# Optimization experiments

Measured on AMD Instinct MI355X. Metric: run time of the kernel, lower is better.

The kernel has to match this reference:

```python
import jax, jax.numpy as jnp
import numpy as np

EPS = 1e-7  # keras backend.epsilon()
NUM_ROUTING = 3


def squash(v, axis=-1):
    s2 = jnp.sum(jnp.square(v), axis=axis, keepdims=True)
    scale = s2 / (1.0 + s2) / jnp.sqrt(s2 + EPS)
    return scale * v


def setup_inputs() -> dict:
    key = jax.random.key(0)
    k1, k2 = jax.random.split(key)
    B, J, I, P, Q = 64, 32, 2048, 32, 16
    inputs = jax.random.normal(k1, (B, I, Q), dtype=jnp.float32)
    # glorot_uniform for W [J, I, P, Q]
    fan_in, fan_out = Q, P
    limit = np.sqrt(6.0 / (fan_in + fan_out))
    W = jax.random.uniform(k2, (J, I, P, Q), dtype=jnp.float32, minval=-limit, maxval=limit)
    return {"inputs": inputs, "W": W}


def reference(inputs, W):
    # prediction vectors: u_hat[b,j,i,p] = sum_q inputs[b,i,q] * W[j,i,p,q]
    inputs_hat = jnp.einsum('biq,jipq->bjip', inputs, W)  # [B,J,I,P]
    inputs_hat_stop = jax.lax.stop_gradient(inputs_hat)
    B, J, I, _ = inputs_hat.shape
    b = jnp.zeros((B, J, I), dtype=inputs_hat.dtype)
    for _ in range(NUM_ROUTING - 1):
        c = jax.nn.softmax(b, axis=1)  # softmax over output capsules j
        v = squash(jnp.einsum('bji,bjip->bjp', c, inputs_hat_stop))
        b = b + jnp.einsum('bjp,bjip->bji', v, inputs_hat_stop)
    c = jax.nn.softmax(b, axis=1)
    return squash(jnp.einsum('bji,bjip->bjp', c, inputs_hat))  # [B,J,P]
```

## Files before the change

### kernel.cpp

```cpp
#include <hip/hip_runtime.h>


namespace {

using bfrag = __attribute__((ext_vector_type(8))) short;
using ffrag = __attribute__((ext_vector_type(4))) float;

constexpr int I_DIM = 2048;
constexpr int B_DIM = 64;
constexpr int N_DIM = 1024;
constexpr int TI    = 16;

__device__ __forceinline__ unsigned short f2bf(float f) {
    unsigned int u = __float_as_uint(f);
    return (unsigned short)((u + 0x7fffu + ((u >> 16) & 1u)) >> 16);
}

template<int CTRL>
__device__ __forceinline__ float dppf(float x) {
    return __int_as_float(
        __builtin_amdgcn_update_dpp(0, __float_as_int(x), CTRL, 0xF, 0xF, true));
}
__device__ __forceinline__ float sum16(float x) {
    x += dppf<0x121>(x); x += dppf<0x122>(x);
    x += dppf<0x124>(x); x += dppf<0x128>(x);
    return x;
}
__device__ __forceinline__ float max16(float x) {
    x = fmaxf(x, dppf<0x121>(x)); x = fmaxf(x, dppf<0x122>(x));
    x = fmaxf(x, dppf<0x124>(x)); x = fmaxf(x, dppf<0x128>(x));
    return x;
}

__device__ __forceinline__ void gl2lds16(const void* gsrc, void* ldst) {
    __builtin_amdgcn_global_load_lds(
        (const __attribute__((address_space(1))) void*)gsrc,
        (__attribute__((address_space(3))) void*)ldst, 16, 0, 0);
}

__device__ __forceinline__ void barrier_lgkm() {
    asm volatile("s_waitcnt lgkmcnt(0)" ::: "memory");
    __builtin_amdgcn_s_barrier();
    __builtin_amdgcn_sched_barrier(0);
}


__global__ __launch_bounds__(256)
void conv_w(const float* __restrict__ W, unsigned short* __restrict__ Wt) {
    const int t = blockIdx.x * 256 + threadIdx.x;
    const int i = t >> 10, n = t & 1023;
    const float* src = W + ((((n >> 5) * I_DIM + i) * 32 + (n & 31)) << 4);
    unsigned int o[8];
    #pragma unroll
    for (int k = 0; k < 8; ++k)
        o[k] = (unsigned int)f2bf(src[2 * k]) | ((unsigned int)f2bf(src[2 * k + 1]) << 16);
    uint4* d0 = reinterpret_cast<uint4*>(Wt + (((size_t)i * 2 + 0) * 1024 + n) * 8);
    uint4* d1 = reinterpret_cast<uint4*>(Wt + (((size_t)i * 2 + 1) * 1024 + n) * 8);
    *d0 = make_uint4(o[0], o[1], o[2], o[3]);
    *d1 = make_uint4(o[4], o[5], o[6], o[7]);
}

__global__ __launch_bounds__(256)
void conv_x(const float* __restrict__ x, unsigned short* __restrict__ xT2) {
    const int t = blockIdx.x * 256 + threadIdx.x;
    const int i = t >> 6, b = t & 63;
    const float* src = x + (((size_t)b * I_DIM + i) << 4);
    unsigned int o[16];
    #pragma unroll
    for (int k = 0; k < 8; ++k) {
        const float f0 = src[2 * k], f1 = src[2 * k + 1];
        const unsigned short h0 = f2bf(f0), h1 = f2bf(f1);
        const float l0 = f0 - __uint_as_float(((unsigned int)h0) << 16);
        const float l1 = f1 - __uint_as_float(((unsigned int)h1) << 16);
        o[k]     = (unsigned int)h0       | ((unsigned int)h1 << 16);
        o[8 + k] = (unsigned int)f2bf(l0) | ((unsigned int)f2bf(l1) << 16);
    }
    #pragma unroll
    for (int g = 0; g < 4; ++g) {
        uint4* dst = reinterpret_cast<uint4*>(xT2 + (((size_t)i * 4 + g) * 64 + b) * 8);
        *dst = make_uint4(o[4 * g], o[4 * g + 1], o[4 * g + 2], o[4 * g + 3]);
    }
}

#define WAITC() do { if (w == 7) asm volatile("s_waitcnt vmcnt(5)" ::: "memory"); \
                     else        asm volatile("s_waitcnt vmcnt(4)" ::: "memory"); } while (0)

template<int ROUTED>
__global__ __launch_bounds__(512, 2)
void caps_fused(const unsigned short* __restrict__ Wt,
                const unsigned short* __restrict__ xT2,
                const float* __restrict__ v_in,
                float* __restrict__ s_out)
{
    __shared__ short wbuf[2][16384];
    __shared__ short xbuf[2][512];
    __shared__ float d_buf[16 * 36];
    __shared__ float c_buf[16 * 36];

    const int tid = threadIdx.x;
    const int w   = tid >> 6;
    const int l   = tid & 63;
    const int g   = l >> 4;
    const int li  = l & 15;
    const int j0  = w << 2;

    const int bid = (int)blockIdx.x;
    const int V   = (bid & 7) * 64 + (bid >> 3);
    const int it  = V >> 2;
    const int b0  = (V & 3) << 4;
    const int i0  = it * TI;

    float vr[4][8];
    if (ROUTED) {
        #pragma unroll
        for (int r = 0; r < 4; ++r)
            #pragma unroll
            for (int t = 0; t < 8; ++t)
                vr[r][t] = v_in[((b0 + (g << 2) + r) * 32 + j0 + (t >> 1)) * 32
                                + ((t & 1) << 4) + li];
        asm volatile("s_waitcnt vmcnt(0)" ::: "memory");
    }

    auto stage = [&](int i, int bufn) {
        const unsigned short* wsrc = Wt + ((size_t)i << 14);
        #pragma unroll
        for (int k = 0; k < 4; ++k) {
            const int c = (w << 2) + k;
            gl2lds16(wsrc + (c << 9) + (l << 3), &wbuf[bufn][c << 9]);
        }
        if (w == 7)
            gl2lds16(xT2 + (((size_t)i << 2) + (l >> 4)) * 512 + ((b0 + (l & 15)) << 3),
                     &xbuf[bufn][0]);
    };

    stage(i0, 0);
    stage(i0 + 1, 1);
    WAITC();
    __builtin_amdgcn_s_barrier();
    __builtin_amdgcn_sched_barrier(0);

    ffrag s[8];
    #pragma unroll
    for (int t = 0; t < 8; ++t) s[t] = ffrag{0.f, 0.f, 0.f, 0.f};

    for (int ii = 0; ii < TI; ++ii) {
        const int cur = ii & 1;

        const bfrag a = *reinterpret_cast<const bfrag*>(&xbuf[cur][((g << 4) + li) << 3]);
        ffrag u[8];
        #pragma unroll
        for (int t = 0; t < 8; ++t) {
            const int n0 = ((j0 + (t >> 1)) << 5) + ((t & 1) << 4);
            const bfrag bt = *reinterpret_cast<const bfrag*>(
                &wbuf[cur][((g & 1) << 13) + ((n0 + li) << 3)]);
            if (ROUTED) {
                ffrag z{0.f, 0.f, 0.f, 0.f};
                u[t] = __builtin_amdgcn_mfma_f32_16x16x32_bf16(a, bt, z, 0, 0, 0);
            } else {
                s[t] = __builtin_amdgcn_mfma_f32_16x16x32_bf16(a, bt, s[t], 0, 0, 0);
            }
        }

        if (ROUTED) {
            #pragma unroll
            for (int r = 0; r < 4; ++r) {
                float d0 = u[0][r] * vr[r][0] + u[1][r] * vr[r][1];
                float d1 = u[2][r] * vr[r][2] + u[3][r] * vr[r][3];
                float d2 = u[4][r] * vr[r][4] + u[5][r] * vr[r][5];
                float d3 = u[6][r] * vr[r][6] + u[7][r] * vr[r][7];
                d0 = sum16(d0); d1 = sum16(d1); d2 = sum16(d2); d3 = sum16(d3);
                float sel = d0;
                sel = (li == 1) ? d1 : sel;
                sel = (li == 2) ? d2 : sel;
                sel = (li == 3) ? d3 : sel;
                if (li < 4) d_buf[((g << 2) + r) * 36 + j0 + li] = sel;
            }
        }
        barrier_lgkm();

        if (ii + 2 < TI) stage(i0 + ii + 2, cur);

        if (ROUTED) {
            const int row = (w << 1) + (l >> 5), jx = l & 31;
            const float dv = d_buf[row * 36 + jx];
            float m = max16(dv);
            m = fmaxf(m, __shfl_xor(m, 16));
            const float e = __expf(dv - m);
            float sm = sum16(e);
            sm += __shfl_xor(sm, 16);
            c_buf[row * 36 + jx] = e / sm;
            barrier_lgkm();

            #pragma unroll
            for (int r = 0; r < 4; ++r) {
                const ffrag cr = *reinterpret_cast<const ffrag*>(
                    &c_buf[((g << 2) + r) * 36 + j0]);
                #pragma unroll
                for (int t = 0; t < 8; ++t)
                    s[t][r] += cr[t >> 1] * u[t][r];
            }
        }

        if (ii + 2 < TI) WAITC();
        else             asm volatile("s_waitcnt vmcnt(0)" ::: "memory");
        __builtin_amdgcn_s_barrier();
        __builtin_amdgcn_sched_barrier(0);
    }

    const float sc = ROUTED ? 1.f : (1.f / 32.f);
    #pragma unroll
    for (int t = 0; t < 8; ++t) {
        const int n0 = ((j0 + (t >> 1)) << 5) + ((t & 1) << 4);
        #pragma unroll
        for (int r = 0; r < 4; ++r)
            atomicAdd(&s_out[(size_t)(b0 + (g << 2) + r) * N_DIM + n0 + li],
                      s[t][r] * sc);
    }
}

__global__ __launch_bounds__(256)
void squash_add(const float* __restrict__ s, const float* __restrict__ base,
                float* __restrict__ dst) {
    const int t = blockIdx.x * 256 + threadIdx.x;
    if (t >= B_DIM * 32) return;
    const float* sp = s + t * 32;
    float n2 = 0.f;
    #pragma unroll
    for (int p = 0; p < 32; ++p) { const float xv = sp[p]; n2 += xv * xv; }
    const float scl = n2 / ((1.f + n2) * sqrtf(n2 + 1e-7f));
    float* op = dst + t * 32;
    #pragma unroll
    for (int p = 0; p < 32; ++p)
        op[p] = (base ? base[t * 32 + p] : 0.f) + scl * sp[p];
}

}

extern "C" void kernel_launch(void* const* d_in, const int* in_sizes, int n_in,
                              void* d_out, int out_size, void* d_ws, size_t ws_size,
                              hipStream_t stream) {
    const float* x = (const float*)d_in[0];
    const float* W = (const float*)d_in[1];
    float* out = (float*)d_out;

    const size_t needW = (size_t)I_DIM * 2 * 1024 * 8 * 2;
    const size_t needX = (size_t)I_DIM * 4 * 64 * 8 * 2;
    const size_t needS = (size_t)B_DIM * N_DIM * 4;

    char* pp = (char*)d_ws;
    unsigned short* Wt  = (unsigned short*)pp; pp += needW;
    unsigned short* xT2 = (unsigned short*)pp; pp += needX;
    float* s  = (float*)pp; pp += needS;
    float* v1 = (float*)pp; pp += needS;
    float* vs = (float*)pp;
    (void)ws_size;

    conv_x<<<(I_DIM * B_DIM) / 256, 256, 0, stream>>>(x, xT2);
    conv_w<<<(I_DIM * N_DIM) / 256, 256, 0, stream>>>(W, Wt);

    const dim3 rg(512), rb(512);

    hipMemsetAsync(s, 0, needS, stream);
    caps_fused<0><<<rg, rb, 0, stream>>>(Wt, xT2, nullptr, s);
    squash_add<<<8, 256, 0, stream>>>(s, nullptr, v1);

    hipMemsetAsync(s, 0, needS, stream);
    caps_fused<1><<<rg, rb, 0, stream>>>(Wt, xT2, v1, s);
    squash_add<<<8, 256, 0, stream>>>(s, v1, vs);

    hipMemsetAsync(s, 0, needS, stream);
    caps_fused<1><<<rg, rb, 0, stream>>>(Wt, xT2, vs, s);
    squash_add<<<8, 256, 0, stream>>>(s, nullptr, out);
}
```

Measured before the change: 286.5 us.

## Use 16-wave blocks with 4-stage LDS ring and software-pipelined routing softmax

Doubles the block to 1024 threads so each wave handles 2 output capsules instead of 4, grows the LDS staging ring from 2 to 4 buffers with 3-ahead prefetch, and double-buffers d_buf/c_buf. The softmax of iteration ii-1 is computed while the MFMAs of iteration ii run, which removes one barrier per iteration in the routed kernel. In exchange, LDS use per block roughly doubles (about 136 KB), which limits occupancy. The launch-bounds hint of 4 blocks per CU is likely unreachable, and the extra barrier participants add synchronisation cost.

```diff
diff --git a/kernel.cpp b/kernel.cpp
--- a/kernel.cpp
+++ b/kernel.cpp
@@ -43,6 +43,11 @@
     __builtin_amdgcn_s_barrier();
     __builtin_amdgcn_sched_barrier(0);
 }
+
+#define WAITC() do {                                                          \
+    if (w == 15) asm volatile("s_waitcnt vmcnt(6)" ::: "memory");             \
+    else         asm volatile("s_waitcnt vmcnt(4)" ::: "memory");             \
+} while (0)
 
 
 __global__ __launch_bounds__(256)
@@ -82,27 +87,24 @@
     }
 }
 
-#define WAITC() do { if (w == 7) asm volatile("s_waitcnt vmcnt(5)" ::: "memory"); \
-                     else        asm volatile("s_waitcnt vmcnt(4)" ::: "memory"); } while (0)
-
 template<int ROUTED>
-__global__ __launch_bounds__(512, 2)
+__global__ __launch_bounds__(1024, 4)
 void caps_fused(const unsigned short* __restrict__ Wt,
                 const unsigned short* __restrict__ xT2,
                 const float* __restrict__ v_in,
                 float* __restrict__ s_out)
 {
-    __shared__ short wbuf[2][16384];
-    __shared__ short xbuf[2][512];
-    __shared__ float d_buf[16 * 36];
-    __shared__ float c_buf[16 * 36];
+    __shared__ __align__(16) short wbuf[4][16384];
+    __shared__ __align__(16) short xbuf[4][512];
+    __shared__ __align__(16) float d_buf[2][16 * 36];
+    __shared__ __align__(16) float c_buf[2][16 * 36];
 
     const int tid = threadIdx.x;
     const int w   = tid >> 6;
     const int l   = tid & 63;
     const int g   = l >> 4;
     const int li  = l & 15;
-    const int j0  = w << 2;
+    const int j0  = w << 1;
 
     const int bid = (int)blockIdx.x;
     const int V   = (bid & 7) * 64 + (bid >> 3);
@@ -110,112 +112,146 @@
     const int b0  = (V & 3) << 4;
     const int i0  = it * TI;
 
-    float vr[4][8];
+    float vr[4][4];
     if (ROUTED) {
         #pragma unroll
         for (int r = 0; r < 4; ++r)
             #pragma unroll
-            for (int t = 0; t < 8; ++t)
+            for (int t = 0; t < 4; ++t)
                 vr[r][t] = v_in[((b0 + (g << 2) + r) * 32 + j0 + (t >> 1)) * 32
                                 + ((t & 1) << 4) + li];
         asm volatile("s_waitcnt vmcnt(0)" ::: "memory");
     }
 
-    auto stage = [&](int i, int bufn) {
+    auto stage = [&](int i, int bn) {
         const unsigned short* wsrc = Wt + ((size_t)i << 14);
         #pragma unroll
-        for (int k = 0; k < 4; ++k) {
-            const int c = (w << 2) + k;
-            gl2lds16(wsrc + (c << 9) + (l << 3), &wbuf[bufn][c << 9]);
-        }
-        if (w == 7)
-            gl2lds16(xT2 + (((size_t)i << 2) + (l >> 4)) * 512 + ((b0 + (l & 15)) << 3),
-                     &xbuf[bufn][0]);
+        for (int k = 0; k < 2; ++k) {
+            const int rr0 = (k << 10) + (w << 6);
+            gl2lds16(wsrc + ((size_t)(rr0 + l) << 3), &wbuf[bn][rr0 << 3]);
+        }
+        if (w == 15)
+            gl2lds16(xT2 + (((size_t)i << 2) + (l >> 4)) * 512
+                         + ((size_t)(b0 + (l & 15)) << 3),
+                     &xbuf[bn][0]);
     };
 
-    stage(i0, 0);
-    stage(i0 + 1, 1);
+    stage(i0, 0); stage(i0 + 1, 1); stage(i0 + 2, 2);
     WAITC();
-    __builtin_amdgcn_s_barrier();
-    __builtin_amdgcn_sched_barrier(0);
-
-    ffrag s[8];
-    #pragma unroll
-    for (int t = 0; t < 8; ++t) s[t] = ffrag{0.f, 0.f, 0.f, 0.f};
-
-    for (int ii = 0; ii < TI; ++ii) {
-        const int cur = ii & 1;
-
-        const bfrag a = *reinterpret_cast<const bfrag*>(&xbuf[cur][((g << 4) + li) << 3]);
-        ffrag u[8];
-        #pragma unroll
-        for (int t = 0; t < 8; ++t) {
-            const int n0 = ((j0 + (t >> 1)) << 5) + ((t & 1) << 4);
-            const bfrag bt = *reinterpret_cast<const bfrag*>(
-                &wbuf[cur][((g & 1) << 13) + ((n0 + li) << 3)]);
-            if (ROUTED) {
-                ffrag z{0.f, 0.f, 0.f, 0.f};
-                u[t] = __builtin_amdgcn_mfma_f32_16x16x32_bf16(a, bt, z, 0, 0, 0);
-            } else {
+    barrier_lgkm();
+
+    ffrag s[4];
+    #pragma unroll
+    for (int t = 0; t < 4; ++t) s[t] = ffrag{0.f, 0.f, 0.f, 0.f};
+
+    if constexpr (!ROUTED) {
+        for (int ii = 0; ii < TI; ++ii) {
+            const int cur4 = ii & 3;
+            const bfrag a = *reinterpret_cast<const bfrag*>(
+                &xbuf[cur4][((g << 4) + li) << 3]);
+            #pragma unroll
+            for (int t = 0; t < 4; ++t) {
+                const int n0 = ((j0 + (t >> 1)) << 5) + ((t & 1) << 4);
+                const bfrag bt = *reinterpret_cast<const bfrag*>(
+                    &wbuf[cur4][((g & 1) << 13) + ((n0 + li) << 3)]);
                 s[t] = __builtin_amdgcn_mfma_f32_16x16x32_bf16(a, bt, s[t], 0, 0, 0);
             }
-        }
-
-        if (ROUTED) {
+            stage(i0 + ((ii + 3 < TI) ? ii + 3 : TI - 1), (ii + 3) & 3);
+            WAITC();
+            barrier_lgkm();
+        }
+    } else {
+        ffrag uA[4], uB[4];
+        #pragma unroll
+        for (int t = 0; t < 4; ++t) uA[t] = ffrag{0.f, 0.f, 0.f, 0.f};
+
+        auto one_iter = [&](int ii, ffrag (&up)[4], ffrag (&un)[4]) {
+            const int cur2 = ii & 1, p2 = cur2 ^ 1, cur4 = ii & 3;
+
+            if (ii > 0 && l < 32) {
+                const float dv = d_buf[p2][w * 36 + l];
+                float m = max16(dv);
+                m = fmaxf(m, __shfl_xor(m, 16));
+                const float e = __expf(dv - m);
+                float sm = sum16(e);
+                sm += __shfl_xor(sm, 16);
+                c_buf[p2][w * 36 + l] = e / sm;
+            }
+
+            const bfrag a = *reinterpret_cast<const bfrag*>(
+                &xbuf[cur4][((g << 4) + li) << 3]);
+            const ffrag z{0.f, 0.f, 0.f, 0.f};
+            #pragma unroll
+            for (int t = 0; t < 4; ++t) {
+                const int n0 = ((j0 + (t >> 1)) << 5) + ((t & 1) << 4);
+                const bfrag bt = *reinterpret_cast<const bfrag*>(
+                    &wbuf[cur4][((g & 1) << 13) + ((n0 + li) << 3)]);
+                un[t] = __builtin_amdgcn_mfma_f32_16x16x32_bf16(a, bt, z, 0, 0, 0);
+            }
+
             #pragma unroll
             for (int r = 0; r < 4; ++r) {
-                float d0 = u[0][r] * vr[r][0] + u[1][r] * vr[r][1];
-                float d1 = u[2][r] * vr[r][2] + u[3][r] * vr[r][3];
-                float d2 = u[4][r] * vr[r][4] + u[5][r] * vr[r][5];
-                float d3 = u[6][r] * vr[r][6] + u[7][r] * vr[r][7];
-                d0 = sum16(d0); d1 = sum16(d1); d2 = sum16(d2); d3 = sum16(d3);
-                float sel = d0;
-                sel = (li == 1) ? d1 : sel;
-                sel = (li == 2) ? d2 : sel;
-                sel = (li == 3) ? d3 : sel;
-                if (li < 4) d_buf[((g << 2) + r) * 36 + j0 + li] = sel;
-            }
-        }
-        barrier_lgkm();
-
-        if (ii + 2 < TI) stage(i0 + ii + 2, cur);
-
-        if (ROUTED) {
-            const int row = (w << 1) + (l >> 5), jx = l & 31;
-            const float dv = d_buf[row * 36 + jx];
+                float d0 = un[0][r] * vr[r][0] + un[1][r] * vr[r][1];
+                float d1 = un[2][r] * vr[r][2] + un[3][r] * vr[r][3];
+                d0 = sum16(d0);
+                d1 = sum16(d1);
+                const float dsel = (li & 1) ? d1 : d0;
+                if (li < 2) d_buf[cur2][((g << 2) + r) * 36 + j0 + li] = dsel;
+            }
+
+            stage(i0 + ((ii + 3 < TI) ? ii + 3 : TI - 1), (ii + 3) & 3);
+
+            WAITC();
+            barrier_lgkm();
+
+            if (ii > 0) {
+                #pragma unroll
+                for (int r = 0; r < 4; ++r) {
+                    const float2 cr = *reinterpret_cast<const float2*>(
+                        &c_buf[p2][((g << 2) + r) * 36 + j0]);
+                    s[0][r] += cr.x * up[0][r];
+                    s[1][r] += cr.x * up[1][r];
+                    s[2][r] += cr.y * up[2][r];
+                    s[3][r] += cr.y * up[3][r];
+                }
+            }
+        };
+
+        for (int cc = 0; cc < TI / 2; ++cc) {
+            one_iter(2 * cc,     uA, uB);
+            one_iter(2 * cc + 1, uB, uA);
+        }
+
+        if (l < 32) {
+            const float dv = d_buf[1][w * 36 + l];
             float m = max16(dv);
             m = fmaxf(m, __shfl_xor(m, 16));
             const float e = __expf(dv - m);
             float sm = sum16(e);
             sm += __shfl_xor(sm, 16);
-            c_buf[row * 36 + jx] = e / sm;
-            barrier_lgkm();
-
-            #pragma unroll
-            for (int r = 0; r < 4; ++r) {
-                const ffrag cr = *reinterpret_cast<const ffrag*>(
-                    &c_buf[((g << 2) + r) * 36 + j0]);
-                #pragma unroll
-                for (int t = 0; t < 8; ++t)
-                    s[t][r] += cr[t >> 1] * u[t][r];
-            }
-        }
-
-        if (ii + 2 < TI) WAITC();
-        else             asm volatile("s_waitcnt vmcnt(0)" ::: "memory");
-        __builtin_amdgcn_s_barrier();
-        __builtin_amdgcn_sched_barrier(0);
+            c_buf[1][w * 36 + l] = e / sm;
+        }
+        barrier_lgkm();
+        #pragma unroll
+        for (int r = 0; r < 4; ++r) {
+            const float2 cr = *reinterpret_cast<const float2*>(
+                &c_buf[1][((g << 2) + r) * 36 + j0]);
+            s[0][r] += cr.x * uA[0][r];
+            s[1][r] += cr.x * uA[1][r];
+            s[2][r] += cr.y * uA[2][r];
+            s[3][r] += cr.y * uA[3][r];
+        }
     }
 
+    asm volatile("s_waitcnt vmcnt(0)" ::: "memory");
     const float sc = ROUTED ? 1.f : (1.f / 32.f);
     #pragma unroll
-    for (int t = 0; t < 8; ++t) {
-        const int n0 = ((j0 + (t >> 1)) << 5) + ((t & 1) << 4);
+    for (int t = 0; t < 4; ++t)
         #pragma unroll
         for (int r = 0; r < 4; ++r)
-            atomicAdd(&s_out[(size_t)(b0 + (g << 2) + r) * N_DIM + n0 + li],
+            atomicAdd(&s_out[(size_t)(b0 + (g << 2) + r) * N_DIM
+                             + ((j0 + (t >> 1)) << 5) + ((t & 1) << 4) + li],
                       s[t][r] * sc);
-    }
 }
 
 __global__ __launch_bounds__(256)
@@ -258,7 +294,7 @@
     conv_x<<<(I_DIM * B_DIM) / 256, 256, 0, stream>>>(x, xT2);
     conv_w<<<(I_DIM * N_DIM) / 256, 256, 0, stream>>>(W, Wt);
 
-    const dim3 rg(512), rb(512);
+    const dim3 rg(512), rb(1024);
 
     hipMemsetAsync(s, 0, needS, stream);
     caps_fused<0><<<rg, rb, 0, stream>>>(Wt, xT2, nullptr, s);
```

Result: faster. 265.3 us (-7.4%).

## Restructure routing kernel: direct global fragment loads, 32-batch tiles, recompute MFMA

Applied to the files above, without the earlier changes.

Replaces the LDS-staged, double-buffered W/x pipeline with direct global loads of bf16 fragments into registers. Uses 1024-thread blocks that each cover 32 batch rows, which halves the grid and reuses each W fragment across two batch groups. Stores the routing vectors v as packed bf16 to save registers, and recomputes the u-hat MFMAs after the softmax instead of keeping them live. The goal is to cut LDS traffic, barrier cost and register pressure, at the price of losing explicit prefetch overlap, doubling MFMA work in the routed passes, and rounding v to bf16.

```diff
diff --git a/kernel.cpp b/kernel.cpp
--- a/kernel.cpp
+++ b/kernel.cpp
@@ -15,6 +15,12 @@
     unsigned int u = __float_as_uint(f);
     return (unsigned short)((u + 0x7fffu + ((u >> 16) & 1u)) >> 16);
 }
+__device__ __forceinline__ float bflo(unsigned int u) {
+    return __uint_as_float(u << 16);
+}
+__device__ __forceinline__ float bfhi(unsigned int u) {
+    return __uint_as_float(u & 0xffff0000u);
+}
 
 template<int CTRL>
 __device__ __forceinline__ float dppf(float x) {
@@ -30,12 +36,6 @@
     x = fmaxf(x, dppf<0x121>(x)); x = fmaxf(x, dppf<0x122>(x));
     x = fmaxf(x, dppf<0x124>(x)); x = fmaxf(x, dppf<0x128>(x));
     return x;
-}
-
-__device__ __forceinline__ void gl2lds16(const void* gsrc, void* ldst) {
-    __builtin_amdgcn_global_load_lds(
-        (const __attribute__((address_space(1))) void*)gsrc,
-        (__attribute__((address_space(3))) void*)ldst, 16, 0, 0);
 }
 
 __device__ __forceinline__ void barrier_lgkm() {
@@ -82,140 +82,135 @@
     }
 }
 
-#define WAITC() do { if (w == 7) asm volatile("s_waitcnt vmcnt(5)" ::: "memory"); \
-                     else        asm volatile("s_waitcnt vmcnt(4)" ::: "memory"); } while (0)
-
 template<int ROUTED>
-__global__ __launch_bounds__(512, 2)
-void caps_fused(const unsigned short* __restrict__ Wt,
+__global__ __launch_bounds__(1024, 4)
+void caps_pass2(const unsigned short* __restrict__ Wt,
                 const unsigned short* __restrict__ xT2,
                 const float* __restrict__ v_in,
                 float* __restrict__ s_out)
 {
-    __shared__ short wbuf[2][16384];
-    __shared__ short xbuf[2][512];
-    __shared__ float d_buf[16 * 36];
-    __shared__ float c_buf[16 * 36];
+    __shared__ float d_buf[32 * 34];
+    __shared__ float c_buf[32 * 34];
 
     const int tid = threadIdx.x;
     const int w   = tid >> 6;
     const int l   = tid & 63;
     const int g   = l >> 4;
     const int li  = l & 15;
-    const int j0  = w << 2;
+    const int j0  = w << 1;
 
     const int bid = (int)blockIdx.x;
-    const int V   = (bid & 7) * 64 + (bid >> 3);
-    const int it  = V >> 2;
-    const int b0  = (V & 3) << 4;
-    const int i0  = it * TI;
-
-    float vr[4][8];
+    const int V   = ((bid & 7) << 5) | (bid >> 3);
+    const int it  = V >> 1;
+    const int bh  = V & 1;
+    const int b0  = bh << 5;
+    const int i0  = it << 4;
+
+    const int aoff = (g << 9) + ((b0 + li) << 3);
+    const int boff = ((g & 1) << 13) + (j0 << 8) + (li << 3);
+
+    unsigned int vr[2][4][2];
     if (ROUTED) {
         #pragma unroll
-        for (int r = 0; r < 4; ++r)
-            #pragma unroll
-            for (int t = 0; t < 8; ++t)
-                vr[r][t] = v_in[((b0 + (g << 2) + r) * 32 + j0 + (t >> 1)) * 32
-                                + ((t & 1) << 4) + li];
-        asm volatile("s_waitcnt vmcnt(0)" ::: "memory");
-    }
-
-    auto stage = [&](int i, int bufn) {
-        const unsigned short* wsrc = Wt + ((size_t)i << 14);
-        #pragma unroll
-        for (int k = 0; k < 4; ++k) {
-            const int c = (w << 2) + k;
-            gl2lds16(wsrc + (c << 9) + (l << 3), &wbuf[bufn][c << 9]);
+        for (int bg = 0; bg < 2; ++bg)
+            #pragma unroll
+            for (int r = 0; r < 4; ++r)
+                #pragma unroll
+                for (int jj = 0; jj < 2; ++jj) {
+                    const int b = b0 + (bg << 4) + (g << 2) + r;
+                    const float* vp = v_in + (((b << 5) + j0 + jj) << 5);
+                    vr[bg][r][jj] = (unsigned int)f2bf(vp[li])
+                                  | ((unsigned int)f2bf(vp[li + 16]) << 16);
+                }
+    }
+
+    ffrag s[2][4];
+    #pragma unroll
+    for (int bg = 0; bg < 2; ++bg)
+        #pragma unroll
+        for (int t = 0; t < 4; ++t) s[bg][t] = ffrag{0.f, 0.f, 0.f, 0.f};
+
+    for (int ii = 0; ii < TI; ++ii) {
+        const int i = i0 + ii;
+        const unsigned short* xa = xT2 + ((size_t)i << 11) + aoff;
+        const unsigned short* xb = Wt + ((size_t)i << 14) + boff;
+        const bfrag A0 = *reinterpret_cast<const bfrag*>(xa);
+        const bfrag A1 = *reinterpret_cast<const bfrag*>(xa + 128);
+        bfrag Bf[4];
+        #pragma unroll
+        for (int t = 0; t < 4; ++t)
+            Bf[t] = *reinterpret_cast<const bfrag*>(xb + ((t >> 1) << 8) + ((t & 1) << 7));
+
+        if constexpr (!ROUTED) {
+            #pragma unroll
+            for (int t = 0; t < 4; ++t) {
+                s[0][t] = __builtin_amdgcn_mfma_f32_16x16x32_bf16(A0, Bf[t], s[0][t], 0, 0, 0);
+                s[1][t] = __builtin_amdgcn_mfma_f32_16x16x32_bf16(A1, Bf[t], s[1][t], 0, 0, 0);
+            }
+        } else {
+            const ffrag z{0.f, 0.f, 0.f, 0.f};
+            #pragma unroll
+            for (int bg = 0; bg < 2; ++bg) {
+                const bfrag a = bg ? A1 : A0;
+                const ffrag u0 = __builtin_amdgcn_mfma_f32_16x16x32_bf16(a, Bf[0], z, 0, 0, 0);
+                const ffrag u1 = __builtin_amdgcn_mfma_f32_16x16x32_bf16(a, Bf[1], z, 0, 0, 0);
+                const ffrag u2 = __builtin_amdgcn_mfma_f32_16x16x32_bf16(a, Bf[2], z, 0, 0, 0);
+                const ffrag u3 = __builtin_amdgcn_mfma_f32_16x16x32_bf16(a, Bf[3], z, 0, 0, 0);
+                #pragma unroll
+                for (int r = 0; r < 4; ++r) {
+                    const unsigned int v0 = vr[bg][r][0], v1 = vr[bg][r][1];
+                    float d0 = u0[r] * bflo(v0) + u1[r] * bfhi(v0);
+                    float d1 = u2[r] * bflo(v1) + u3[r] * bfhi(v1);
+                    d0 = sum16(d0);
+                    d1 = sum16(d1);
+                    const float dsel = (li & 1) ? d1 : d0;
+                    if (li < 2)
+                        d_buf[((bg << 4) + (g << 2) + r) * 34 + j0 + li] = dsel;
+                }
+            }
+            barrier_lgkm();
+
+            {
+                const int bl = tid >> 5, jx = tid & 31;
+                const float dv = d_buf[bl * 34 + jx];
+                float m = max16(dv);
+                m = fmaxf(m, __shfl_xor(m, 16));
+                const float e = __expf(dv - m);
+                float sm = sum16(e);
+                sm += __shfl_xor(sm, 16);
+                c_buf[bl * 34 + jx] = e / sm;
+            }
+            barrier_lgkm();
+
+            #pragma unroll
+            for (int bg = 0; bg < 2; ++bg) {
+                const bfrag a = bg ? A1 : A0;
+                float2 c2[4];
+                #pragma unroll
+                for (int r = 0; r < 4; ++r)
+                    c2[r] = *reinterpret_cast<const float2*>(
+                        &c_buf[((bg << 4) + (g << 2) + r) * 34 + j0]);
+                #pragma unroll
+                for (int t = 0; t < 4; ++t) {
+                    const ffrag u = __builtin_amdgcn_mfma_f32_16x16x32_bf16(a, Bf[t], z, 0, 0, 0);
+                    #pragma unroll
+                    for (int r = 0; r < 4; ++r)
+                        s[bg][t][r] += ((t >> 1) ? c2[r].y : c2[r].x) * u[r];
+                }
+            }
         }
-        if (w == 7)
-            gl2lds16(xT2 + (((size_t)i << 2) + (l >> 4)) * 512 + ((b0 + (l & 15)) << 3),
-                     &xbuf[bufn][0]);
-    };
-
-    stage(i0, 0);
-    stage(i0 + 1, 1);
-    WAITC();
-    __builtin_amdgcn_s_barrier();
-    __builtin_amdgcn_sched_barrier(0);
-
-    ffrag s[8];
-    #pragma unroll
-    for (int t = 0; t < 8; ++t) s[t] = ffrag{0.f, 0.f, 0.f, 0.f};
-
-    for (int ii = 0; ii < TI; ++ii) {
-        const int cur = ii & 1;
-
-        const bfrag a = *reinterpret_cast<const bfrag*>(&xbuf[cur][((g << 4) + li) << 3]);
-        ffrag u[8];
-        #pragma unroll
-        for (int t = 0; t < 8; ++t) {
-            const int n0 = ((j0 + (t >> 1)) << 5) + ((t & 1) << 4);
-            const bfrag bt = *reinterpret_cast<const bfrag*>(
-                &wbuf[cur][((g & 1) << 13) + ((n0 + li) << 3)]);
-            if (ROUTED) {
-                ffrag z{0.f, 0.f, 0.f, 0.f};
-                u[t] = __builtin_amdgcn_mfma_f32_16x16x32_bf16(a, bt, z, 0, 0, 0);
-            } else {
-                s[t] = __builtin_amdgcn_mfma_f32_16x16x32_bf16(a, bt, s[t], 0, 0, 0);
-            }
-        }
-
-        if (ROUTED) {
-            #pragma unroll
-            for (int r = 0; r < 4; ++r) {
-                float d0 = u[0][r] * vr[r][0] + u[1][r] * vr[r][1];
-                float d1 = u[2][r] * vr[r][2] + u[3][r] * vr[r][3];
-                float d2 = u[4][r] * vr[r][4] + u[5][r] * vr[r][5];
-                float d3 = u[6][r] * vr[r][6] + u[7][r] * vr[r][7];
-                d0 = sum16(d0); d1 = sum16(d1); d2 = sum16(d2); d3 = sum16(d3);
-                float sel = d0;
-                sel = (li == 1) ? d1 : sel;
-                sel = (li == 2) ? d2 : sel;
-                sel = (li == 3) ? d3 : sel;
-                if (li < 4) d_buf[((g << 2) + r) * 36 + j0 + li] = sel;
-            }
-        }
-        barrier_lgkm();
-
-        if (ii + 2 < TI) stage(i0 + ii + 2, cur);
-
-        if (ROUTED) {
-            const int row = (w << 1) + (l >> 5), jx = l & 31;
-            const float dv = d_buf[row * 36 + jx];
-            float m = max16(dv);
-            m = fmaxf(m, __shfl_xor(m, 16));
-            const float e = __expf(dv - m);
-            float sm = sum16(e);
-            sm += __shfl_xor(sm, 16);
-            c_buf[row * 36 + jx] = e / sm;
-            barrier_lgkm();
-
-            #pragma unroll
-            for (int r = 0; r < 4; ++r) {
-                const ffrag cr = *reinterpret_cast<const ffrag*>(
-                    &c_buf[((g << 2) + r) * 36 + j0]);
-                #pragma unroll
-                for (int t = 0; t < 8; ++t)
-                    s[t][r] += cr[t >> 1] * u[t][r];
-            }
-        }
-
-        if (ii + 2 < TI) WAITC();
-        else             asm volatile("s_waitcnt vmcnt(0)" ::: "memory");
-        __builtin_amdgcn_s_barrier();
-        __builtin_amdgcn_sched_barrier(0);
     }
 
     const float sc = ROUTED ? 1.f : (1.f / 32.f);
     #pragma unroll
-    for (int t = 0; t < 8; ++t) {
-        const int n0 = ((j0 + (t >> 1)) << 5) + ((t & 1) << 4);
-        #pragma unroll
-        for (int r = 0; r < 4; ++r)
-            atomicAdd(&s_out[(size_t)(b0 + (g << 2) + r) * N_DIM + n0 + li],
-                      s[t][r] * sc);
-    }
+    for (int bg = 0; bg < 2; ++bg)
+        #pragma unroll
+        for (int t = 0; t < 4; ++t)
+            #pragma unroll
+            for (int r = 0; r < 4; ++r)
+                atomicAdd(&s_out[(size_t)(b0 + (bg << 4) + (g << 2) + r) * N_DIM
+                                 + ((j0 + (t >> 1)) << 5) + ((t & 1) << 4) + li],
+                          s[bg][t][r] * sc);
 }
 
 __global__ __launch_bounds__(256)
@@ -258,17 +253,17 @@
     conv_x<<<(I_DIM * B_DIM) / 256, 256, 0, stream>>>(x, xT2);
     conv_w<<<(I_DIM * N_DIM) / 256, 256, 0, stream>>>(W, Wt);
 
-    const dim3 rg(512), rb(512);
+    const dim3 rg(256), rb(1024);
 
     hipMemsetAsync(s, 0, needS, stream);
-    caps_fused<0><<<rg, rb, 0, stream>>>(Wt, xT2, nullptr, s);
+    caps_pass2<0><<<rg, rb, 0, stream>>>(Wt, xT2, nullptr, s);
     squash_add<<<8, 256, 0, stream>>>(s, nullptr, v1);
 
     hipMemsetAsync(s, 0, needS, stream);
-    caps_fused<1><<<rg, rb, 0, stream>>>(Wt, xT2, v1, s);
+    caps_pass2<1><<<rg, rb, 0, stream>>>(Wt, xT2, v1, s);
     squash_add<<<8, 256, 0, stream>>>(s, v1, vs);
 
     hipMemsetAsync(s, 0, needS, stream);
-    caps_fused<1><<<rg, rb, 0, stream>>>(Wt, xT2, vs, s);
+    caps_pass2<1><<<rg, rb, 0, stream>>>(Wt, xT2, vs, s);
     squash_add<<<8, 256, 0, stream>>>(s, nullptr, out);
 }
```

Result: no change. 290.5 us (+1.4%).
